# Kernel tuning notes

Hardware: AMD Instinct MI355X
Metric: run time of the kernel (lower is better)

Reference implementation:

```python
import jax, jax.numpy as jnp
import numpy as np

B, T, V, H = 32, 256, 16, 256


def _layer_norm(x, g, b, eps=1e-5):
    m = jnp.mean(x, axis=-1, keepdims=True)
    v = jnp.mean(jnp.square(x - m), axis=-1, keepdims=True)
    return (x - m) * jax.lax.rsqrt(v + eps) * g + b


def setup_inputs() -> dict:
    keys = iter(jax.random.split(jax.random.key(0), 16))

    def nrm(shape, s=0.02):
        return (jax.random.normal(next(keys), shape, dtype=jnp.float32) * s).astype(jnp.float32)

    return {
        "x": nrm((B, T, V, H), 1.0),
        "context": nrm((B, T, H), 1.0),
        "joint_Wa": nrm((V * H, H)),
        "joint_ba": jnp.zeros((H,), jnp.float32),
        "joint_Wc": nrm((H, H)),
        "joint_Wi": nrm((H, H)),
        "joint_bi": jnp.zeros((H,), jnp.float32),
        "joint_Wglu": nrm((H, 2 * V)),
        "joint_bglu": jnp.zeros((2 * V,), jnp.float32),
        "joint_Wskip": nrm((V * H, V)),
        "joint_bskip": jnp.zeros((V,), jnp.float32),
        "joint_ln_g": jnp.ones((V,), jnp.float32),
        "joint_ln_b": jnp.zeros((V,), jnp.float32),
        "var_Wa": nrm((V, H, H)),
        "var_ba": jnp.zeros((V, H), jnp.float32),
        "var_Wi": nrm((V, H, H)),
        "var_bi": jnp.zeros((V, H), jnp.float32),
        "var_Wglu": nrm((V, H, 2 * H)),
        "var_bglu": jnp.zeros((V, 2 * H), jnp.float32),
        "var_ln_g": jnp.ones((V, H), jnp.float32),
        "var_ln_b": jnp.zeros((V, H), jnp.float32),
    }


def reference(x, context, joint_Wa, joint_ba, joint_Wc, joint_Wi, joint_bi,
              joint_Wglu, joint_bglu, joint_Wskip, joint_bskip,
              joint_ln_g, joint_ln_b,
              var_Wa, var_ba, var_Wi, var_bi, var_Wglu, var_bglu,
              var_ln_g, var_ln_b):
    b, t, v, h = x.shape
    Xi = x.reshape(b, t, v * h)  # flatten last two dims

    # ---- joint GRN (with context) producing variable logits [b,t,v] ----
    a = Xi @ joint_Wa + joint_ba + context @ joint_Wc
    a = jax.nn.elu(a)
    i = a @ joint_Wi + joint_bi
    g = i @ joint_Wglu + joint_bglu
    g1, g2 = jnp.split(g, 2, axis=-1)  # GLU: first half gated by sigmoid(second)
    glu_out = g1 * jax.nn.sigmoid(g2)
    skip = Xi @ joint_Wskip + joint_bskip  # out_size != in_size -> skip projection
    sparse_weights = jax.nn.softmax(_layer_norm(glu_out + skip, joint_ln_g, joint_ln_b), axis=-1)

    # ---- per-variable GRNs, batched over the variable axis ----
    av = jax.nn.elu(jnp.einsum('btvh,vhk->btvk', x, var_Wa) + var_ba)
    iv = jnp.einsum('btvh,vhk->btvk', av, var_Wi) + var_bi
    gv = jnp.einsum('btvh,vhd->btvd', iv, var_Wglu) + var_bglu
    gv1, gv2 = jnp.split(gv, 2, axis=-1)
    tv = _layer_norm(gv1 * jax.nn.sigmoid(gv2) + x, var_ln_g, var_ln_b)  # [b,t,v,h]

    # stack(dim=-1) + matmul with weights == weighted sum over variables
    variable_ctx = jnp.einsum('btvh,btv->bth', tv, sparse_weights)
    return variable_ctx, sparse_weights
```

## Files before the change

### kernel.cpp

```cpp
#include <hip/hip_runtime.h>

typedef unsigned short u16;
typedef __attribute__((ext_vector_type(8))) __bf16 bf16x8;
typedef __attribute__((ext_vector_type(4))) float f32x4;
typedef __attribute__((ext_vector_type(8))) u16 u16x8;

__device__ __forceinline__ u16 f2b(float f) {
  union { float f; unsigned u; } v; v.f = f;
  return (u16)((v.u + 0x7fffu + ((v.u >> 16) & 1u)) >> 16);
}
__device__ __forceinline__ float b2f(u16 h) {
  union { unsigned u; float f; } v; v.u = ((unsigned)h) << 16;
  return v.f;
}
__device__ __forceinline__ f32x4 mfma16(bf16x8 a, bf16x8 b, f32x4 c) {
  return __builtin_amdgcn_mfma_f32_16x16x32_bf16(a, b, c, 0, 0, 0);
}
__device__ __forceinline__ void gl_lds16(const void* g, void* l) {
  __builtin_amdgcn_global_load_lds(
      (const __attribute__((address_space(1))) void*)g,
      (__attribute__((address_space(3))) void*)l, 16, 0, 0);
}
__device__ __forceinline__ u16x8 cvt8(float4 a, float4 b) {
  u16x8 o;
  o[0] = f2b(a.x); o[1] = f2b(a.y); o[2] = f2b(a.z); o[3] = f2b(a.w);
  o[4] = f2b(b.x); o[5] = f2b(b.y); o[6] = f2b(b.z); o[7] = f2b(b.w);
  return o;
}

__global__ __launch_bounds__(256) void transpose_cast(
    const float* __restrict__ src, u16* __restrict__ dst,
    int R, int C, int dstStride, long srcBatch, long dstBatch)
{
  __shared__ float tile[32][33];
  src += (long)blockIdx.z * srcBatch;
  dst += (long)blockIdx.z * dstBatch;
  const int c0 = blockIdx.x * 32, r0 = blockIdx.y * 32;
  const int tx = threadIdx.x & 31, ty = threadIdx.x >> 5;
  for (int i = ty; i < 32; i += 8) {
    int r = r0 + i, cc = c0 + tx;
    if (r < R && cc < C) tile[i][tx] = src[(long)r * C + cc];
  }
  __syncthreads();
  for (int i = ty; i < 32; i += 8) {
    int cc = c0 + i, r = r0 + tx;
    if (cc < C && r < R) dst[(long)cc * dstStride + r] = f2b(tile[tx][i]);
  }
}

__global__ __launch_bounds__(256) void var_w_prep(
    const float* __restrict__ W, u16* __restrict__ dstbase, int rbase)
{
  const int v = blockIdx.x;
  const int kc = blockIdx.y;
  const int n = threadIdx.x;
  const float* src = W + (size_t)v * 65536 + (size_t)kc * 64 * 256 + n;
  u16* dst = dstbase + (size_t)v * 262144 + (size_t)(rbase + kc) * 16384;
#pragma unroll
  for (int l = 0; l < 8; ++l) {
    u16x8 o;
#pragma unroll
    for (int e = 0; e < 8; ++e) o[e] = f2b(src[(l * 8 + e) * 256]);
    const int chunk = n * 8 + (l ^ (n & 7));
    *(u16x8*)&dst[chunk * 8] = o;
  }
}

__global__ __launch_bounds__(256) void var_wglu_prep(
    const float* __restrict__ W, u16* __restrict__ dstbase)
{
  const int v = blockIdx.x;
  const int kc = blockIdx.y;
  u16* dst = dstbase + (size_t)v * 262144 + (size_t)(8 + kc) * 16384;
#pragma unroll
  for (int half = 0; half < 2; ++half) {
    const int n = threadIdx.x + half * 256;
    const float* src = W + (size_t)v * 131072 + (size_t)kc * 32 * 512 + n;
    const int s = n >> 1;
#pragma unroll
    for (int l = 0; l < 4; ++l) {
      u16x8 o;
#pragma unroll
      for (int e = 0; e < 8; ++e) o[e] = f2b(src[(l * 8 + e) * 512]);
      const int chunk = s * 8 + ((((n & 1) * 4 + l)) ^ (s & 7));
      *(u16x8*)&dst[chunk * 8] = o;
    }
  }
}

#define K1TOT 4352
__global__ __launch_bounds__(256, 3) void gemm1(
    const float* __restrict__ x, const float* __restrict__ ctx,
    const u16* __restrict__ bt1, const float* __restrict__ ba,
    const float* __restrict__ bskip, u16* __restrict__ a_bf, float* __restrict__ skip_f)
{
  __shared__ u16 As[32 * 64];
  __shared__ u16 Bs[288 * 64];
  const int tid = threadIdx.x;
  const int n0 = blockIdx.x * 32;
  const int w = tid >> 6, lane = tid & 63;
  const int q = lane >> 4, c = lane & 15;
  const int rt = w & 1, cg = w >> 1;
  const int t0 = cg ? 9 : 0;
  const int nt = cg ? 8 : 9;

  f32x4 acc[9];
#pragma unroll
  for (int i = 0; i < 9; ++i) acc[i] = f32x4{0.f, 0.f, 0.f, 0.f};

  const int sr = tid >> 3, sp = tid & 7;
  const int sl = sp ^ (sr & 7);

  for (int kb = 0; kb < K1TOT; kb += 64) {
    {
      const float* s = (kb < 4096)
          ? (x + (size_t)(n0 + sr) * 4096 + kb + sl * 8)
          : (ctx + (size_t)(n0 + sr) * 256 + (kb - 4096) + sl * 8);
      float4 v0 = ((const float4*)s)[0];
      float4 v1 = ((const float4*)s)[1];
      *(u16x8*)&As[tid * 8] = cvt8(v0, v1);
    }
#pragma unroll
    for (int i = 0; i < 9; ++i) {
      const int cb = (i * 4 + w) * 64;
      const int cid = cb + lane;
      const int row = cid >> 3, p = cid & 7;
      const int l = p ^ (row & 7);
      const u16* src = (row < 272) ? (bt1 + (size_t)row * K1TOT + kb + l * 8) : bt1;
      gl_lds16(src, &Bs[cb * 8]);
    }
    __syncthreads();
#pragma unroll
    for (int kk = 0; kk < 2; ++kk) {
      const int arow = rt * 16 + c;
      bf16x8 af = *(const bf16x8*)&As[(arow * 64 + kk * 32 + q * 8) ^ ((arow & 7) << 3)];
#pragma unroll
      for (int ti = 0; ti < 9; ++ti) {
        if (ti < nt) {
          const int n16 = (t0 + ti) * 16 + c;
          bf16x8 bfr = *(const bf16x8*)&Bs[(n16 * 64 + kk * 32 + q * 8) ^ ((n16 & 7) << 3)];
          acc[ti] = mfma16(af, bfr, acc[ti]);
        }
      }
    }
    __syncthreads();
  }
#pragma unroll
  for (int ti = 0; ti < 9; ++ti) {
    if (ti < nt) {
      const int col = (t0 + ti) * 16 + c;
#pragma unroll
      for (int j = 0; j < 4; ++j) {
        const long n = n0 + rt * 16 + q * 4 + j;
        float vv = acc[ti][j];
        if (col < 256) {
          vv += ba[col];
          vv = vv > 0.f ? vv : expm1f(vv);
          a_bf[n * 256 + col] = f2b(vv);
        } else {
          skip_f[n * 16 + (col - 256)] = vv + bskip[col - 256];
        }
      }
    }
  }
}

__global__ __launch_bounds__(256, 3) void gemm_i(
    const u16* __restrict__ a_bf, const u16* __restrict__ wiT,
    const float* __restrict__ bi, u16* __restrict__ i_bf)
{
  __shared__ u16 As[32 * 64];
  __shared__ u16 Bs[256 * 64];
  const int tid = threadIdx.x;
  const int n0 = blockIdx.x * 32;
  const int w = tid >> 6, lane = tid & 63;
  const int q = lane >> 4, c = lane & 15;
  const int rt = w & 1, cg = w >> 1;

  f32x4 acc[8];
#pragma unroll
  for (int i = 0; i < 8; ++i) acc[i] = f32x4{0.f, 0.f, 0.f, 0.f};

  for (int kb = 0; kb < 256; kb += 64) {
    {
      const int row = tid >> 3, p = tid & 7;
      const int l = p ^ (row & 7);
      gl_lds16(a_bf + (size_t)(n0 + row) * 256 + kb + l * 8, &As[w * 512]);
    }
#pragma unroll
    for (int i = 0; i < 8; ++i) {
      const int cb = (i * 4 + w) * 64;
      const int cid = cb + lane;
      const int row = cid >> 3, p = cid & 7;
      const int l = p ^ (row & 7);
      gl_lds16(wiT + (size_t)row * 256 + kb + l * 8, &Bs[cb * 8]);
    }
    __syncthreads();
#pragma unroll
    for (int kk = 0; kk < 2; ++kk) {
      const int arow = rt * 16 + c;
      bf16x8 af = *(const bf16x8*)&As[(arow * 64 + kk * 32 + q * 8) ^ ((arow & 7) << 3)];
#pragma unroll
      for (int ti = 0; ti < 8; ++ti) {
        const int n16 = (cg * 8 + ti) * 16 + c;
        bf16x8 bfr = *(const bf16x8*)&Bs[(n16 * 64 + kk * 32 + q * 8) ^ ((n16 & 7) << 3)];
        acc[ti] = mfma16(af, bfr, acc[ti]);
      }
    }
    __syncthreads();
  }
#pragma unroll
  for (int ti = 0; ti < 8; ++ti) {
    const int col = (cg * 8 + ti) * 16 + c;
    const float bb = bi[col];
#pragma unroll
    for (int j = 0; j < 4; ++j) {
      const long n = n0 + rt * 16 + q * 4 + j;
      i_bf[n * 256 + col] = f2b(acc[ti][j] + bb);
    }
  }
}

__global__ __launch_bounds__(256) void joint_tail(
    const u16* __restrict__ i_bf, const u16* __restrict__ wgluT,
    const float* __restrict__ bglu, const float* __restrict__ skip_f,
    const float* __restrict__ lng, const float* __restrict__ lnb,
    float* __restrict__ swout)
{
  __shared__ float wlds[32 * 257];
  __shared__ float ilds[4][256];
  const int tid = threadIdx.x;
  for (int jj = 0; jj < 32; ++jj) wlds[jj * 257 + tid] = b2f(wgluT[jj * 256 + tid]);
  const int w = tid >> 6, lane = tid & 63;
  const long n = (long)blockIdx.x * 4 + w;
  {
    const u16* src = i_bf + n * 256 + lane * 4;
    float4 f;
    f.x = b2f(src[0]); f.y = b2f(src[1]); f.z = b2f(src[2]); f.w = b2f(src[3]);
    *(float4*)&ilds[w][lane * 4] = f;
  }
  __syncthreads();
  const int cc32 = lane & 31;
  const int k0 = (lane >> 5) * 128;
  float acc = 0.f;
  for (int k = 0; k < 128; ++k) acc += ilds[w][k0 + k] * wlds[cc32 * 257 + k0 + k];
  acc += __shfl_xor(acc, 32, 64);
  const float gfull = acc + bglu[cc32];
  const int cc = lane & 15;
  const float g1 = __shfl(gfull, cc, 64);
  const float g2 = __shfl(gfull, cc + 16, 64);
  const float glu = g1 / (1.f + __expf(-g2));
  const float y = glu + skip_f[n * 16 + cc];
  float s = y, ss = y * y;
#pragma unroll
  for (int d = 1; d < 16; d <<= 1) { s += __shfl_xor(s, d, 64); ss += __shfl_xor(ss, d, 64); }
  const float m = s * (1.f / 16.f);
  const float var = ss * (1.f / 16.f) - m * m;
  const float t = (y - m) * rsqrtf(var + 1e-5f) * lng[cc] + lnb[cc];
  float mx = t;
#pragma unroll
  for (int d = 1; d < 16; d <<= 1) mx = fmaxf(mx, __shfl_xor(mx, d, 64));
  const float e = __expf(t - mx);
  float es = e;
#pragma unroll
  for (int d = 1; d < 16; d <<= 1) es += __shfl_xor(es, d, 64);
  if (lane < 16) swout[n * 16 + lane] = e / es;
}

__global__ __launch_bounds__(512, 4) void var_chain(
    const float* __restrict__ x, const u16* __restrict__ varw,
    const float* __restrict__ vba, const float* __restrict__ vbi,
    const float* __restrict__ vbglu, const float* __restrict__ vlng,
    const float* __restrict__ vlnb, const float* __restrict__ sw,
    float* __restrict__ out)
{
  extern __shared__ u16 smem[];
  u16* const xt1 = smem;
  u16* const wt  = smem + 16384;
  float* const red   = (float*)(smem + 32768);
  float* const muinv = red + 1024;

  const int tid = threadIdx.x;
  const int w = tid >> 6, lane = tid & 63;
  const int q = lane >> 4, c = lane & 15;
  const int rt0 = (w & 1) << 1, cg = w >> 1;
  const int vbase = blockIdx.x * 4;
  const int n0 = blockIdx.y * 64;

  f32x4 outacc[4][2];
#pragma unroll
  for (int p = 0; p < 4; ++p)
#pragma unroll
    for (int u = 0; u < 2; ++u) outacc[p][u] = f32x4{0.f, 0.f, 0.f, 0.f};

  for (int vi = 0; vi < 4; ++vi) {
    const int v = vbase + vi;
    const u16* vtiles = varw + (size_t)v * 262144;

#pragma unroll
    for (int jj = 0; jj < 4; ++jj) {
      const int cid = jj * 512 + tid;
      const int r = cid >> 5, p = cid & 31;
      const int l = (p & 24) | ((p & 7) ^ (r & 7));
      const float* s = x + (size_t)(n0 + r) * 4096 + (size_t)v * 256 + l * 8;
      float4 v0 = ((const float4*)s)[0];
      float4 v1 = ((const float4*)s)[1];
      *(u16x8*)&xt1[cid * 8] = cvt8(v0, v1);
    }
    __syncthreads();

    f32x4 acc2[2][4];
#pragma unroll
    for (int p = 0; p < 2; ++p)
#pragma unroll
      for (int ti = 0; ti < 4; ++ti) acc2[p][ti] = f32x4{0.f, 0.f, 0.f, 0.f};

    for (int kc = 0; kc < 4; ++kc) {
      {
        const u16* tb = vtiles + (size_t)kc * 16384;
#pragma unroll
        for (int i = 0; i < 4; ++i) {
          const int cb = (i * 8 + w) * 64;
          gl_lds16(tb + (size_t)(cb + lane) * 8, wt + (size_t)cb * 8);
        }
      }
      __syncthreads();
#pragma unroll
      for (int kk = 0; kk < 2; ++kk) {
        const int r0 = rt0 * 16 + c, r1 = (rt0 + 1) * 16 + c;
        bf16x8 a0 = *(const bf16x8*)&xt1[(r0 * 256 + kc * 64 + kk * 32 + q * 8) ^ ((r0 & 7) << 3)];
        bf16x8 a1 = *(const bf16x8*)&xt1[(r1 * 256 + kc * 64 + kk * 32 + q * 8) ^ ((r1 & 7) << 3)];
#pragma unroll
        for (int ti = 0; ti < 4; ++ti) {
          const int n16 = (cg * 4 + ti) * 16 + c;
          bf16x8 b = *(const bf16x8*)&wt[(n16 * 64 + kk * 32 + q * 8) ^ ((n16 & 7) << 3)];
          acc2[0][ti] = mfma16(a0, b, acc2[0][ti]);
          acc2[1][ti] = mfma16(a1, b, acc2[1][ti]);
        }
      }
      __syncthreads();
    }
#pragma unroll
    for (int p = 0; p < 2; ++p)
#pragma unroll
      for (int ti = 0; ti < 4; ++ti) {
        const int col = (cg * 4 + ti) * 16 + c;
        const float bb = vba[v * 256 + col];
#pragma unroll
        for (int j = 0; j < 4; ++j) {
          const int row = (rt0 + p) * 16 + q * 4 + j;
          float vv = acc2[p][ti][j] + bb;
          vv = vv > 0.f ? vv : expm1f(vv);
          xt1[(row * 256 + col) ^ ((row & 7) << 3)] = f2b(vv);
        }
      }
    __syncthreads();

#pragma unroll
    for (int p = 0; p < 2; ++p)
#pragma unroll
      for (int ti = 0; ti < 4; ++ti) acc2[p][ti] = f32x4{0.f, 0.f, 0.f, 0.f};
    for (int kc = 0; kc < 4; ++kc) {
      {
        const u16* tb = vtiles + (size_t)(4 + kc) * 16384;
#pragma unroll
        for (int i = 0; i < 4; ++i) {
          const int cb = (i * 8 + w) * 64;
          gl_lds16(tb + (size_t)(cb + lane) * 8, wt + (size_t)cb * 8);
        }
      }
      __syncthreads();
#pragma unroll
      for (int kk = 0; kk < 2; ++kk) {
        const int r0 = rt0 * 16 + c, r1 = (rt0 + 1) * 16 + c;
        bf16x8 a0 = *(const bf16x8*)&xt1[(r0 * 256 + kc * 64 + kk * 32 + q * 8) ^ ((r0 & 7) << 3)];
        bf16x8 a1 = *(const bf16x8*)&xt1[(r1 * 256 + kc * 64 + kk * 32 + q * 8) ^ ((r1 & 7) << 3)];
#pragma unroll
        for (int ti = 0; ti < 4; ++ti) {
          const int n16 = (cg * 4 + ti) * 16 + c;
          bf16x8 b = *(const bf16x8*)&wt[(n16 * 64 + kk * 32 + q * 8) ^ ((n16 & 7) << 3)];
          acc2[0][ti] = mfma16(a0, b, acc2[0][ti]);
          acc2[1][ti] = mfma16(a1, b, acc2[1][ti]);
        }
      }
      __syncthreads();
    }
#pragma unroll
    for (int p = 0; p < 2; ++p)
#pragma unroll
      for (int ti = 0; ti < 4; ++ti) {
        const int col = (cg * 4 + ti) * 16 + c;
        const float bb = vbi[v * 256 + col];
#pragma unroll
        for (int j = 0; j < 4; ++j) {
          const int row = (rt0 + p) * 16 + q * 4 + j;
          xt1[(row * 256 + col) ^ ((row & 7) << 3)] = f2b(acc2[p][ti][j] + bb);
        }
      }
    __syncthreads();

    f32x4 acc3[4][4];
#pragma unroll
    for (int p = 0; p < 4; ++p)
#pragma unroll
      for (int u = 0; u < 4; ++u) acc3[p][u] = f32x4{0.f, 0.f, 0.f, 0.f};
    for (int kc = 0; kc < 8; ++kc) {
      {
        const u16* tb = vtiles + (size_t)(8 + kc) * 16384;
#pragma unroll
        for (int i = 0; i < 4; ++i) {
          const int cb = (i * 8 + w) * 64;
          gl_lds16(tb + (size_t)(cb + lane) * 8, wt + (size_t)cb * 8);
        }
      }
      __syncthreads();
      bf16x8 a[4];
#pragma unroll
      for (int p = 0; p < 4; ++p) {
        const int r = p * 16 + c;
        a[p] = *(const bf16x8*)&xt1[(r * 256 + kc * 32 + q * 8) ^ ((r & 7) << 3)];
      }
#pragma unroll
      for (int u = 0; u < 4; ++u) {
        const int gt = 2 * w + (u & 1) + (u >> 1) * 16;
        const int n = gt * 16 + c;
        const int idx = (n >> 1) * 64 + ((((n & 1) * 4 + q) ^ ((n >> 1) & 7)) * 8);
        bf16x8 b = *(const bf16x8*)&wt[idx];
#pragma unroll
        for (int p = 0; p < 4; ++p) acc3[p][u] = mfma16(a[p], b, acc3[p][u]);
      }
      __syncthreads();
    }

    float b1v[2], b2v[2], lgv[2], lbv[2];
#pragma unroll
    for (int u01 = 0; u01 < 2; ++u01) {
      const int col = w * 32 + u01 * 16 + c;
      b1v[u01] = vbglu[v * 512 + col];
      b2v[u01] = vbglu[v * 512 + 256 + col];
      lgv[u01] = vlng[v * 256 + col];
      lbv[u01] = vlnb[v * 256 + col];
    }
    float rs[4][4], rss[4][4];
#pragma unroll
    for (int p = 0; p < 4; ++p)
#pragma unroll
      for (int j = 0; j < 4; ++j) { rs[p][j] = 0.f; rss[p][j] = 0.f; }
#pragma unroll
    for (int h = 0; h < 2; ++h) {
      float resid[2][2][4];
#pragma unroll
      for (int pp = 0; pp < 2; ++pp)
#pragma unroll
        for (int u01 = 0; u01 < 2; ++u01) {
          const int col = w * 32 + u01 * 16 + c;
#pragma unroll
          for (int j = 0; j < 4; ++j) {
            const int row = (h * 2 + pp) * 16 + q * 4 + j;
            resid[pp][u01][j] = x[(size_t)(n0 + row) * 4096 + (size_t)v * 256 + col];
          }
        }
#pragma unroll
      for (int pp = 0; pp < 2; ++pp) {
        const int p = h * 2 + pp;
#pragma unroll
        for (int u01 = 0; u01 < 2; ++u01) {
#pragma unroll
          for (int j = 0; j < 4; ++j) {
            const float g1 = acc3[p][u01][j] + b1v[u01];
            const float g2 = acc3[p][u01 + 2][j] + b2v[u01];
            const float glu = g1 / (1.f + __expf(-g2));
            const float r = glu + resid[pp][u01][j];
            acc3[p][u01][j] = r;
            rs[p][j] += r; rss[p][j] += r * r;
          }
        }
      }
    }
#pragma unroll
    for (int p = 0; p < 4; ++p)
#pragma unroll
      for (int j = 0; j < 4; ++j)
#pragma unroll
        for (int d = 1; d < 16; d <<= 1) {
          rs[p][j]  += __shfl_xor(rs[p][j], d, 64);
          rss[p][j] += __shfl_xor(rss[p][j], d, 64);
        }
    if (c == 0) {
#pragma unroll
      for (int p = 0; p < 4; ++p)
#pragma unroll
        for (int j = 0; j < 4; ++j) {
          const int row = p * 16 + q * 4 + j;
          red[row * 16 + w * 2]     = rs[p][j];
          red[row * 16 + w * 2 + 1] = rss[p][j];
        }
    }
    __syncthreads();
    if (tid < 64) {
      float ms = 0.f, vs = 0.f;
#pragma unroll
      for (int ww = 0; ww < 8; ++ww) { ms += red[tid * 16 + ww * 2]; vs += red[tid * 16 + ww * 2 + 1]; }
      const float mm = ms * (1.f / 256.f);
      muinv[tid * 2]     = mm;
      muinv[tid * 2 + 1] = rsqrtf(vs * (1.f / 256.f) - mm * mm + 1e-5f);
    }
    __syncthreads();
#pragma unroll
    for (int p = 0; p < 4; ++p) {
#pragma unroll
      for (int j = 0; j < 4; ++j) {
        const int row = p * 16 + q * 4 + j;
        const float mu = muinv[row * 2], inv = muinv[row * 2 + 1];
        const float wv = sw[(size_t)(n0 + row) * 16 + v];
#pragma unroll
        for (int u01 = 0; u01 < 2; ++u01) {
          const float tv = (acc3[p][u01][j] - mu) * inv * lgv[u01] + lbv[u01];
          outacc[p][u01][j] += tv * wv;
        }
      }
    }
    __syncthreads();
  }

#pragma unroll
  for (int p = 0; p < 4; ++p)
#pragma unroll
    for (int u01 = 0; u01 < 2; ++u01) {
      const int col = w * 32 + u01 * 16 + c;
#pragma unroll
      for (int j = 0; j < 4; ++j) {
        const int row = p * 16 + q * 4 + j;
        atomicAdd(&out[(size_t)(n0 + row) * 256 + col], outacc[p][u01][j]);
      }
    }
}

extern "C" void kernel_launch(void* const* d_in, const int* in_sizes, int n_in,
                              void* d_out, int out_size, void* d_ws, size_t ws_size,
                              hipStream_t stream) {
  const float* x     = (const float*)d_in[0];
  const float* ctx   = (const float*)d_in[1];
  const float* jWa   = (const float*)d_in[2];
  const float* jba   = (const float*)d_in[3];
  const float* jWc   = (const float*)d_in[4];
  const float* jWi   = (const float*)d_in[5];
  const float* jbi   = (const float*)d_in[6];
  const float* jWglu = (const float*)d_in[7];
  const float* jbglu = (const float*)d_in[8];
  const float* jWskip= (const float*)d_in[9];
  const float* jbskip= (const float*)d_in[10];
  const float* jlng  = (const float*)d_in[11];
  const float* jlnb  = (const float*)d_in[12];
  const float* vWa   = (const float*)d_in[13];
  const float* vba   = (const float*)d_in[14];
  const float* vWi   = (const float*)d_in[15];
  const float* vbi   = (const float*)d_in[16];
  const float* vWglu = (const float*)d_in[17];
  const float* vbglu = (const float*)d_in[18];
  const float* vlng  = (const float*)d_in[19];
  const float* vlnb  = (const float*)d_in[20];
  float* out = (float*)d_out;

  char* ws = (char*)d_ws;
  size_t off = 0;
  auto alloc = [&](size_t bytes) { void* p = ws + off; off += (bytes + 255) & ~(size_t)255; return p; };
  u16* bt1     = (u16*)alloc((size_t)272 * 4352 * 2);
  u16* wiT     = (u16*)alloc((size_t)256 * 256 * 2);
  u16* wgluT   = (u16*)alloc((size_t)32 * 256 * 2);
  u16* varw    = (u16*)alloc((size_t)16 * 262144 * 2);
  u16* a_bf    = (u16*)alloc((size_t)8192 * 256 * 2);
  u16* i_bf    = (u16*)alloc((size_t)8192 * 256 * 2);
  float* skipf = (float*)alloc((size_t)8192 * 16 * 4);

  hipMemsetAsync(bt1, 0, (size_t)272 * 4352 * 2, stream);
  hipMemsetAsync(out, 0, (size_t)8192 * 256 * 4, stream);

  dim3 blk(256);
  transpose_cast<<<dim3(8, 128, 1),  blk, 0, stream>>>(jWa,   bt1,              4096, 256, 4352, 0, 0);
  transpose_cast<<<dim3(8, 8, 1),    blk, 0, stream>>>(jWc,   bt1 + 4096,       256,  256, 4352, 0, 0);
  transpose_cast<<<dim3(1, 128, 1),  blk, 0, stream>>>(jWskip,bt1 + 256 * 4352, 4096, 16,  4352, 0, 0);
  transpose_cast<<<dim3(8, 8, 1),    blk, 0, stream>>>(jWi,   wiT,   256, 256, 256, 0, 0);
  transpose_cast<<<dim3(1, 8, 1),    blk, 0, stream>>>(jWglu, wgluT, 256, 32,  256, 0, 0);
  var_w_prep<<<dim3(16, 4), blk, 0, stream>>>(vWa, varw, 0);
  var_w_prep<<<dim3(16, 4), blk, 0, stream>>>(vWi, varw, 4);
  var_wglu_prep<<<dim3(16, 8), blk, 0, stream>>>(vWglu, varw);

  gemm1<<<dim3(256), blk, 0, stream>>>(x, ctx, bt1, jba, jbskip, a_bf, skipf);
  gemm_i<<<dim3(256), blk, 0, stream>>>(a_bf, wiT, jbi, i_bf);
  joint_tail<<<dim3(2048), blk, 0, stream>>>(i_bf, wgluT, jbglu, skipf, jlng, jlnb,
                                             out + (size_t)8192 * 256);

  hipFuncSetAttribute((const void*)var_chain, hipFuncAttributeMaxDynamicSharedMemorySize, 70144);
  var_chain<<<dim3(4, 128), dim3(512), 70144, stream>>>(x, varw, vba, vbi, vbglu,
                                                        vlng, vlnb,
                                                        out + (size_t)8192 * 256, out);
}
```

Measured before the change: 526.4 us.

## Double-buffer var_chain weight tiles and double the row tile to 128

The per-variable GRN kernel now uses 1024-thread blocks that each handle 128 rows instead of 64. Weight tiles are double-buffered in LDS so the async global-to-LDS load of the next tile overlaps the MFMA work on the current one, with one barrier per tile instead of two. Reusing each staged weight tile across twice as many rows halves weight traffic per output, and the warp layout changes to 4 row groups by 4 column groups. In exchange, LDS use roughly doubles to about 136 KB, so only one block fits per CU, and the grid halves to 256 blocks, which may leave the device under-filled.

```diff
diff --git a/kernel.cpp b/kernel.cpp
--- a/kernel.cpp
+++ b/kernel.cpp
@@ -267,7 +267,7 @@
   if (lane < 16) swout[n * 16 + lane] = e / es;
 }
 
-__global__ __launch_bounds__(512, 4) void var_chain(
+__global__ __launch_bounds__(1024, 1) void var_chain(
     const float* __restrict__ x, const u16* __restrict__ varw,
     const float* __restrict__ vba, const float* __restrict__ vbi,
     const float* __restrict__ vbglu, const float* __restrict__ vlng,
@@ -276,30 +276,43 @@
 {
   extern __shared__ u16 smem[];
   u16* const xt1 = smem;
-  u16* const wt  = smem + 16384;
-  float* const red   = (float*)(smem + 32768);
+  u16* const wtb = smem + 32768;
+  float* const red   = (float*)(smem + 65536);
   float* const muinv = red + 1024;
 
   const int tid = threadIdx.x;
   const int w = tid >> 6, lane = tid & 63;
   const int q = lane >> 4, c = lane & 15;
-  const int rt0 = (w & 1) << 1, cg = w >> 1;
+  const int rt = w >> 2, cg = w & 3;
   const int vbase = blockIdx.x * 4;
-  const int n0 = blockIdx.y * 64;
-
-  f32x4 outacc[4][2];
-#pragma unroll
-  for (int p = 0; p < 4; ++p)
-#pragma unroll
-    for (int u = 0; u < 2; ++u) outacc[p][u] = f32x4{0.f, 0.f, 0.f, 0.f};
+  const int n0 = blockIdx.y * 128;
+
+  f32x4 outacc[2][4];
+#pragma unroll
+  for (int p = 0; p < 2; ++p)
+#pragma unroll
+    for (int u = 0; u < 4; ++u) outacc[p][u] = f32x4{0.f, 0.f, 0.f, 0.f};
+
+  auto STAGE = [&](int b, int tn) {
+    const u16* tb = varw + (size_t)(vbase + (tn >> 4)) * 262144 + (size_t)(tn & 15) * 16384;
+    u16* dst = wtb + (b << 14);
+#pragma unroll
+    for (int i = 0; i < 2; ++i) {
+      const int cb = (i * 16 + w) * 64;
+      gl_lds16(tb + (size_t)(cb + lane) * 8, dst + (size_t)cb * 8);
+    }
+  };
+
+  int cur = 0;
+  STAGE(0, 0);
 
   for (int vi = 0; vi < 4; ++vi) {
     const int v = vbase + vi;
-    const u16* vtiles = varw + (size_t)v * 262144;
+    const int tb0 = vi * 16;
 
 #pragma unroll
     for (int jj = 0; jj < 4; ++jj) {
-      const int cid = jj * 512 + tid;
+      const int cid = jj * 1024 + tid;
       const int r = cid >> 5, p = cid & 31;
       const int l = (p & 24) | ((p & 7) ^ (r & 7));
       const float* s = x + (size_t)(n0 + r) * 4096 + (size_t)v * 256 + l * 8;
@@ -315,30 +328,29 @@
 #pragma unroll
       for (int ti = 0; ti < 4; ++ti) acc2[p][ti] = f32x4{0.f, 0.f, 0.f, 0.f};
 
-    for (int kc = 0; kc < 4; ++kc) {
-      {
-        const u16* tb = vtiles + (size_t)kc * 16384;
-#pragma unroll
-        for (int i = 0; i < 4; ++i) {
-          const int cb = (i * 8 + w) * 64;
-          gl_lds16(tb + (size_t)(cb + lane) * 8, wt + (size_t)cb * 8);
-        }
-      }
-      __syncthreads();
+    for (int t = tb0; t < tb0 + 4; ++t) {
+      const int tn = t + 1 < 64 ? t + 1 : 63;
+      STAGE(cur ^ 1, tn);
+      const u16* wcur = wtb + (cur << 14);
+      const int kc = t - tb0;
 #pragma unroll
       for (int kk = 0; kk < 2; ++kk) {
-        const int r0 = rt0 * 16 + c, r1 = (rt0 + 1) * 16 + c;
-        bf16x8 a0 = *(const bf16x8*)&xt1[(r0 * 256 + kc * 64 + kk * 32 + q * 8) ^ ((r0 & 7) << 3)];
-        bf16x8 a1 = *(const bf16x8*)&xt1[(r1 * 256 + kc * 64 + kk * 32 + q * 8) ^ ((r1 & 7) << 3)];
+        bf16x8 a[2];
+#pragma unroll
+        for (int p = 0; p < 2; ++p) {
+          const int r = (rt * 2 + p) * 16 + c;
+          a[p] = *(const bf16x8*)&xt1[(r * 256 + kc * 64 + kk * 32 + q * 8) ^ ((r & 7) << 3)];
+        }
 #pragma unroll
         for (int ti = 0; ti < 4; ++ti) {
           const int n16 = (cg * 4 + ti) * 16 + c;
-          bf16x8 b = *(const bf16x8*)&wt[(n16 * 64 + kk * 32 + q * 8) ^ ((n16 & 7) << 3)];
-          acc2[0][ti] = mfma16(a0, b, acc2[0][ti]);
-          acc2[1][ti] = mfma16(a1, b, acc2[1][ti]);
+          bf16x8 b = *(const bf16x8*)&wcur[(n16 * 64 + kk * 32 + q * 8) ^ ((n16 & 7) << 3)];
+          acc2[0][ti] = mfma16(a[0], b, acc2[0][ti]);
+          acc2[1][ti] = mfma16(a[1], b, acc2[1][ti]);
         }
       }
       __syncthreads();
+      cur ^= 1;
     }
 #pragma unroll
     for (int p = 0; p < 2; ++p)
@@ -348,7 +360,7 @@
         const float bb = vba[v * 256 + col];
 #pragma unroll
         for (int j = 0; j < 4; ++j) {
-          const int row = (rt0 + p) * 16 + q * 4 + j;
+          const int row = (rt * 2 + p) * 16 + q * 4 + j;
           float vv = acc2[p][ti][j] + bb;
           vv = vv > 0.f ? vv : expm1f(vv);
           xt1[(row * 256 + col) ^ ((row & 7) << 3)] = f2b(vv);
@@ -360,30 +372,29 @@
     for (int p = 0; p < 2; ++p)
 #pragma unroll
       for (int ti = 0; ti < 4; ++ti) acc2[p][ti] = f32x4{0.f, 0.f, 0.f, 0.f};
-    for (int kc = 0; kc < 4; ++kc) {
-      {
-        const u16* tb = vtiles + (size_t)(4 + kc) * 16384;
-#pragma unroll
-        for (int i = 0; i < 4; ++i) {
-          const int cb = (i * 8 + w) * 64;
-          gl_lds16(tb + (size_t)(cb + lane) * 8, wt + (size_t)cb * 8);
-        }
-      }
-      __syncthreads();
+    for (int t = tb0 + 4; t < tb0 + 8; ++t) {
+      const int tn = t + 1 < 64 ? t + 1 : 63;
+      STAGE(cur ^ 1, tn);
+      const u16* wcur = wtb + (cur << 14);
+      const int kc = t - (tb0 + 4);
 #pragma unroll
       for (int kk = 0; kk < 2; ++kk) {
-        const int r0 = rt0 * 16 + c, r1 = (rt0 + 1) * 16 + c;
-        bf16x8 a0 = *(const bf16x8*)&xt1[(r0 * 256 + kc * 64 + kk * 32 + q * 8) ^ ((r0 & 7) << 3)];
-        bf16x8 a1 = *(const bf16x8*)&xt1[(r1 * 256 + kc * 64 + kk * 32 + q * 8) ^ ((r1 & 7) << 3)];
+        bf16x8 a[2];
+#pragma unroll
+        for (int p = 0; p < 2; ++p) {
+          const int r = (rt * 2 + p) * 16 + c;
+          a[p] = *(const bf16x8*)&xt1[(r * 256 + kc * 64 + kk * 32 + q * 8) ^ ((r & 7) << 3)];
+        }
 #pragma unroll
         for (int ti = 0; ti < 4; ++ti) {
           const int n16 = (cg * 4 + ti) * 16 + c;
-          bf16x8 b = *(const bf16x8*)&wt[(n16 * 64 + kk * 32 + q * 8) ^ ((n16 & 7) << 3)];
-          acc2[0][ti] = mfma16(a0, b, acc2[0][ti]);
-          acc2[1][ti] = mfma16(a1, b, acc2[1][ti]);
+          bf16x8 b = *(const bf16x8*)&wcur[(n16 * 64 + kk * 32 + q * 8) ^ ((n16 & 7) << 3)];
+          acc2[0][ti] = mfma16(a[0], b, acc2[0][ti]);
+          acc2[1][ti] = mfma16(a[1], b, acc2[1][ti]);
         }
       }
       __syncthreads();
+      cur ^= 1;
     }
 #pragma unroll
     for (int p = 0; p < 2; ++p)
@@ -393,92 +404,73 @@
         const float bb = vbi[v * 256 + col];
 #pragma unroll
         for (int j = 0; j < 4; ++j) {
-          const int row = (rt0 + p) * 16 + q * 4 + j;
+          const int row = (rt * 2 + p) * 16 + q * 4 + j;
           xt1[(row * 256 + col) ^ ((row & 7) << 3)] = f2b(acc2[p][ti][j] + bb);
         }
       }
     __syncthreads();
 
-    f32x4 acc3[4][4];
-#pragma unroll
-    for (int p = 0; p < 4; ++p)
-#pragma unroll
-      for (int u = 0; u < 4; ++u) acc3[p][u] = f32x4{0.f, 0.f, 0.f, 0.f};
-    for (int kc = 0; kc < 8; ++kc) {
-      {
-        const u16* tb = vtiles + (size_t)(8 + kc) * 16384;
-#pragma unroll
-        for (int i = 0; i < 4; ++i) {
-          const int cb = (i * 8 + w) * 64;
-          gl_lds16(tb + (size_t)(cb + lane) * 8, wt + (size_t)cb * 8);
-        }
+    f32x4 acc3[2][8];
+#pragma unroll
+    for (int p = 0; p < 2; ++p)
+#pragma unroll
+      for (int u = 0; u < 8; ++u) acc3[p][u] = f32x4{0.f, 0.f, 0.f, 0.f};
+    for (int t = tb0 + 8; t < tb0 + 16; ++t) {
+      const int tn = t + 1 < 64 ? t + 1 : 63;
+      STAGE(cur ^ 1, tn);
+      const u16* wcur = wtb + (cur << 14);
+      const int kc = t - (tb0 + 8);
+      bf16x8 a[2];
+#pragma unroll
+      for (int p = 0; p < 2; ++p) {
+        const int r = (rt * 2 + p) * 16 + c;
+        a[p] = *(const bf16x8*)&xt1[(r * 256 + kc * 32 + q * 8) ^ ((r & 7) << 3)];
+      }
+#pragma unroll
+      for (int u = 0; u < 8; ++u) {
+        const int ct = cg * 4 + (u & 3) + ((u >> 2) << 4);
+        const int n = ct * 16 + c;
+        const int idx = (n >> 1) * 64 + ((((n & 1) * 4 + q) ^ ((n >> 1) & 7)) * 8);
+        bf16x8 b = *(const bf16x8*)&wcur[idx];
+        acc3[0][u] = mfma16(a[0], b, acc3[0][u]);
+        acc3[1][u] = mfma16(a[1], b, acc3[1][u]);
       }
       __syncthreads();
-      bf16x8 a[4];
-#pragma unroll
-      for (int p = 0; p < 4; ++p) {
-        const int r = p * 16 + c;
-        a[p] = *(const bf16x8*)&xt1[(r * 256 + kc * 32 + q * 8) ^ ((r & 7) << 3)];
-      }
+      cur ^= 1;
+    }
+
+    float b1v[4], b2v[4], lgv[4], lbv[4];
+#pragma unroll
+    for (int u = 0; u < 4; ++u) {
+      const int col = cg * 64 + u * 16 + c;
+      b1v[u] = vbglu[v * 512 + col];
+      b2v[u] = vbglu[v * 512 + 256 + col];
+      lgv[u] = vlng[v * 256 + col];
+      lbv[u] = vlnb[v * 256 + col];
+    }
+    float rs[2][4], rss[2][4];
+#pragma unroll
+    for (int p = 0; p < 2; ++p)
+#pragma unroll
+      for (int j = 0; j < 4; ++j) { rs[p][j] = 0.f; rss[p][j] = 0.f; }
+#pragma unroll
+    for (int p = 0; p < 2; ++p)
 #pragma unroll
       for (int u = 0; u < 4; ++u) {
-        const int gt = 2 * w + (u & 1) + (u >> 1) * 16;
-        const int n = gt * 16 + c;
-        const int idx = (n >> 1) * 64 + ((((n & 1) * 4 + q) ^ ((n >> 1) & 7)) * 8);
-        bf16x8 b = *(const bf16x8*)&wt[idx];
-#pragma unroll
-        for (int p = 0; p < 4; ++p) acc3[p][u] = mfma16(a[p], b, acc3[p][u]);
-      }
-      __syncthreads();
-    }
-
-    float b1v[2], b2v[2], lgv[2], lbv[2];
-#pragma unroll
-    for (int u01 = 0; u01 < 2; ++u01) {
-      const int col = w * 32 + u01 * 16 + c;
-      b1v[u01] = vbglu[v * 512 + col];
-      b2v[u01] = vbglu[v * 512 + 256 + col];
-      lgv[u01] = vlng[v * 256 + col];
-      lbv[u01] = vlnb[v * 256 + col];
-    }
-    float rs[4][4], rss[4][4];
-#pragma unroll
-    for (int p = 0; p < 4; ++p)
-#pragma unroll
-      for (int j = 0; j < 4; ++j) { rs[p][j] = 0.f; rss[p][j] = 0.f; }
-#pragma unroll
-    for (int h = 0; h < 2; ++h) {
-      float resid[2][2][4];
-#pragma unroll
-      for (int pp = 0; pp < 2; ++pp)
-#pragma unroll
-        for (int u01 = 0; u01 < 2; ++u01) {
-          const int col = w * 32 + u01 * 16 + c;
-#pragma unroll
-          for (int j = 0; j < 4; ++j) {
-            const int row = (h * 2 + pp) * 16 + q * 4 + j;
-            resid[pp][u01][j] = x[(size_t)(n0 + row) * 4096 + (size_t)v * 256 + col];
-          }
-        }
-#pragma unroll
-      for (int pp = 0; pp < 2; ++pp) {
-        const int p = h * 2 + pp;
-#pragma unroll
-        for (int u01 = 0; u01 < 2; ++u01) {
-#pragma unroll
-          for (int j = 0; j < 4; ++j) {
-            const float g1 = acc3[p][u01][j] + b1v[u01];
-            const float g2 = acc3[p][u01 + 2][j] + b2v[u01];
-            const float glu = g1 / (1.f + __expf(-g2));
-            const float r = glu + resid[pp][u01][j];
-            acc3[p][u01][j] = r;
-            rs[p][j] += r; rss[p][j] += r * r;
-          }
-        }
-      }
-    }
-#pragma unroll
-    for (int p = 0; p < 4; ++p)
+        const int col = cg * 64 + u * 16 + c;
+#pragma unroll
+        for (int j = 0; j < 4; ++j) {
+          const int row = (rt * 2 + p) * 16 + q * 4 + j;
+          const float g1 = acc3[p][u][j] + b1v[u];
+          const float g2 = acc3[p][u + 4][j] + b2v[u];
+          const float glu = g1 / (1.f + __expf(-g2));
+          const float r = glu + x[(size_t)(n0 + row) * 4096 + (size_t)v * 256 + col];
+          acc3[p][u][j] = r;
+          rs[p][j] += r; rss[p][j] += r * r;
+        }
+      }
+#pragma unroll
+    for (int p = 0; p < 2; ++p)
 #pragma unroll
       for (int j = 0; j < 4; ++j)
 #pragma unroll
@@ -488,50 +480,50 @@
         }
     if (c == 0) {
 #pragma unroll
-      for (int p = 0; p < 4; ++p)
+      for (int p = 0; p < 2; ++p)
 #pragma unroll
         for (int j = 0; j < 4; ++j) {
-          const int row = p * 16 + q * 4 + j;
-          red[row * 16 + w * 2]     = rs[p][j];
-          red[row * 16 + w * 2 + 1] = rss[p][j];
-        }
-    }
-    __syncthreads();
-    if (tid < 64) {
+          const int row = (rt * 2 + p) * 16 + q * 4 + j;
+          red[row * 8 + cg * 2]     = rs[p][j];
+          red[row * 8 + cg * 2 + 1] = rss[p][j];
+        }
+    }
+    __syncthreads();
+    if (tid < 128) {
       float ms = 0.f, vs = 0.f;
 #pragma unroll
-      for (int ww = 0; ww < 8; ++ww) { ms += red[tid * 16 + ww * 2]; vs += red[tid * 16 + ww * 2 + 1]; }
+      for (int ww = 0; ww < 4; ++ww) { ms += red[tid * 8 + ww * 2]; vs += red[tid * 8 + ww * 2 + 1]; }
       const float mm = ms * (1.f / 256.f);
       muinv[tid * 2]     = mm;
       muinv[tid * 2 + 1] = rsqrtf(vs * (1.f / 256.f) - mm * mm + 1e-5f);
     }
     __syncthreads();
 #pragma unroll
-    for (int p = 0; p < 4; ++p) {
+    for (int p = 0; p < 2; ++p) {
 #pragma unroll
       for (int j = 0; j < 4; ++j) {
-        const int row = p * 16 + q * 4 + j;
+        const int row = (rt * 2 + p) * 16 + q * 4 + j;
         const float mu = muinv[row * 2], inv = muinv[row * 2 + 1];
         const float wv = sw[(size_t)(n0 + row) * 16 + v];
 #pragma unroll
-        for (int u01 = 0; u01 < 2; ++u01) {
-          const float tv = (acc3[p][u01][j] - mu) * inv * lgv[u01] + lbv[u01];
-          outacc[p][u01][j] += tv * wv;
-        }
-      }
-    }
-    __syncthreads();
-  }
-
-#pragma unroll
-  for (int p = 0; p < 4; ++p)
-#pragma unroll
-    for (int u01 = 0; u01 < 2; ++u01) {
-      const int col = w * 32 + u01 * 16 + c;
+        for (int u = 0; u < 4; ++u) {
+          const float tv = (acc3[p][u][j] - mu) * inv * lgv[u] + lbv[u];
+          outacc[p][u][j] += tv * wv;
+        }
+      }
+    }
+    __syncthreads();
+  }
+
+#pragma unroll
+  for (int p = 0; p < 2; ++p)
+#pragma unroll
+    for (int u = 0; u < 4; ++u) {
+      const int col = cg * 64 + u * 16 + c;
 #pragma unroll
       for (int j = 0; j < 4; ++j) {
-        const int row = p * 16 + q * 4 + j;
-        atomicAdd(&out[(size_t)(n0 + row) * 256 + col], outacc[p][u01][j]);
+        const int row = (rt * 2 + p) * 16 + q * 4 + j;
+        atomicAdd(&out[(size_t)(n0 + row) * 256 + col], outacc[p][u][j]);
       }
     }
 }
@@ -591,8 +583,8 @@
   joint_tail<<<dim3(2048), blk, 0, stream>>>(i_bf, wgluT, jbglu, skipf, jlng, jlnb,
                                              out + (size_t)8192 * 256);
 
-  hipFuncSetAttribute((const void*)var_chain, hipFuncAttributeMaxDynamicSharedMemorySize, 70144);
-  var_chain<<<dim3(4, 128), dim3(512), 70144, stream>>>(x, varw, vba, vbi, vbglu,
-                                                        vlng, vlnb,
-                                                        out + (size_t)8192 * 256, out);
-}
+  hipFuncSetAttribute((const void*)var_chain, hipFuncAttributeMaxDynamicSharedMemorySize, 136192);
+  var_chain<<<dim3(4, 64), dim3(1024), 136192, stream>>>(x, varw, vba, vbi, vbglu,
+                                                         vlng, vlnb,
+                                                         out + (size_t)8192 * 256, out);
+}
```

Measured after the change: 479.3 us. 8.9% less time.
